# Kernel optimization log

Measured on AMD Instinct MI355X. Metric: run time of the kernel, lower is better.

## Reference

```python
import jax, jax.numpy as jnp
import numpy as np

N = 100_000   # nodes
E = 1_600_000 # edges
F_IN = 128
H = 128
C = 16


def setup_inputs() -> dict:
    key = jax.random.key(0)
    ks = jax.random.split(key, 11)
    s = 0.05
    return {
        "x": jax.random.normal(ks[0], (N, F_IN), jnp.float32),
        "edge_index": jax.random.randint(ks[1], (2, E), 0, N, jnp.int32),
        "edge_weight": jax.random.uniform(ks[2], (E,), jnp.float32),
        # first_lin: Linear(features_num, hidden)
        "W_first": jax.random.normal(ks[3], (F_IN, H), jnp.float32) * s,
        "b_first": jax.random.normal(ks[4], (H,), jnp.float32) * s,
        # two GCNConv(hidden, hidden) layers (num_layers - 1 = 2)
        "W_conv1": jax.random.normal(ks[5], (H, H), jnp.float32) * s,
        "b_conv1": jax.random.normal(ks[6], (H,), jnp.float32) * s,
        "W_conv2": jax.random.normal(ks[7], (H, H), jnp.float32) * s,
        "b_conv2": jax.random.normal(ks[8], (H,), jnp.float32) * s,
        # lin2: Linear(hidden, num_class)
        "W_out": jax.random.normal(ks[9], (H, C), jnp.float32) * s,
        "b_out": jax.random.normal(ks[10], (C,), jnp.float32) * s,
    }


def reference(x, edge_index, edge_weight, W_first, b_first,
              W_conv1, b_conv1, W_conv2, b_conv2, W_out, b_out):
    src, dst = edge_index[0], edge_index[1]

    # first_lin + relu (dropout p=0.8 is identity at inference)
    h = jax.nn.relu(x @ W_first + b_first)

    # GCN normalization with self-loops (fill weight 1.0), shared across layers
    deg = jax.ops.segment_sum(edge_weight, dst, num_segments=N) + 1.0
    dinv = jax.lax.rsqrt(deg)                      # [N]
    norm = dinv[src] * edge_weight * dinv[dst]     # [E]
    self_norm = dinv * dinv                        # [N], self-loop contribution

    for W, b in ((W_conv1, b_conv1), (W_conv2, b_conv2)):
        hw = h @ W                                  # [N, H]
        msgs = hw[src] * norm[:, None]              # [E, H] gather + scale
        agg = jax.ops.segment_sum(msgs, dst, num_segments=N)
        agg = agg + hw * self_norm[:, None]         # self-loop term
        h = jax.nn.relu(agg + b)

    # dropout p=0.5 identity at inference; final linear
    return h @ W_out + b_out
```

## Files before the change

kernel.cpp:

```cpp
#include <hip/hip_runtime.h>

typedef unsigned short u16;
typedef unsigned int u32;
using bf16x8 = __attribute__((ext_vector_type(8))) short;
using f32x4  = __attribute__((ext_vector_type(4))) float;

#define SLOT 64
#define NSHARD 128
#define SHMASK 127
#define SHBITS 7
#define QRT 4
#define SPQ 16
#define LDSN 782
#define CB 256
#define OVF_CAP 131072

static __device__ __forceinline__ u16 f2bf(float f) {
    u32 u = __float_as_uint(f);
    u = (u + 0x7fffu + ((u >> 16) & 1u)) >> 16;
    return (u16)u;
}
static __device__ __forceinline__ float bf2f(u16 h) {
    return __uint_as_float(((u32)h) << 16);
}
static __device__ __forceinline__ float pk_w(u32 e) {
    return (float)(int)((e & 0x7fffu) - 1u) * (1.0f / 32766.0f);
}
static __device__ __forceinline__ size_t nodeBase(int d) {
    return ((size_t)((d & SHMASK) * LDSN + (d >> SHBITS))) << 6;
}

__global__ void k_prep(const float* __restrict__ Wf, const float* __restrict__ W1,
                       const float* __restrict__ W2, u16* __restrict__ wfrag) {
    const float* W = (blockIdx.x == 0) ? Wf : (blockIdx.x == 1 ? W1 : W2);
    u16* o = wfrag + (size_t)blockIdx.x * 16384;
    for (int fid = threadIdx.x; fid < 2048; fid += 256) {
        int c = fid & 15, g = (fid >> 4) & 3, kk = (fid >> 6) & 3, ct = fid >> 8;
        const float* wp = W + (size_t)(kk * 32 + g * 8) * 128 + ct * 16 + c;
        bf16x8 pv;
#pragma unroll
        for (int j = 0; j < 8; ++j) pv[j] = (short)f2bf(wp[(size_t)j * 128]);
        *(bf16x8*)&o[(size_t)fid * 8] = pv;
    }
}

__global__ __launch_bounds__(256) void k_part1(const int* __restrict__ dst,
                                               int* __restrict__ cnt, int E, int CH) {
    __shared__ int lc[NSHARD];
    for (int i = threadIdx.x; i < NSHARD; i += 256) lc[i] = 0;
    __syncthreads();
    int e0 = blockIdx.x * CH, e1 = min(E, e0 + CH);
    for (int e = e0 + (int)threadIdx.x; e < e1; e += 256)
        atomicAdd(&lc[dst[e] & SHMASK], 1);
    __syncthreads();
    for (int i = threadIdx.x; i < NSHARD; i += 256)
        cnt[blockIdx.x * NSHARD + i] = lc[i];
}

__global__ __launch_bounds__(256) void k_scan_a(const int* __restrict__ cnt,
                                                int* __restrict__ offs,
                                                int* __restrict__ tot) {
    __shared__ int sd[256];
    int s = blockIdx.x, t = threadIdx.x;
    int v = cnt[t * NSHARD + s];
    sd[t] = v;
    __syncthreads();
    for (int off = 1; off < 256; off <<= 1) {
        int x = (t >= off) ? sd[t - off] : 0;
        __syncthreads();
        sd[t] += x;
        __syncthreads();
    }
    offs[s * CB + t] = sd[t] - v;
    if (t == 255) tot[s] = sd[255];
}

__global__ void k_scan_b(const int* __restrict__ tot, int* __restrict__ base, int E) {
    __shared__ int sd[NSHARD];
    int t = threadIdx.x;
    int v = tot[t];
    sd[t] = v;
    __syncthreads();
    for (int off = 1; off < NSHARD; off <<= 1) {
        int x = (t >= off) ? sd[t - off] : 0;
        __syncthreads();
        sd[t] += x;
        __syncthreads();
    }
    base[t] = sd[t] - v;
    if (t == NSHARD - 1) base[NSHARD] = E;
}

template <bool AF32, bool RELU_BIAS>
static __device__ __forceinline__ void gemm_body(
    int bid, const void* __restrict__ Araw, const u16* __restrict__ Wfrag,
    const float* __restrict__ bias, u16* __restrict__ C, int n)
{
    const int t = threadIdx.x;
    const int lane = t & 63;
    const int wave = t >> 6;
    const int rowbase = bid * 128 + wave * 32;
    const int lrow = lane & 15;
    const int g = lane >> 4;

    bf16x8 a[2][4];
#pragma unroll
    for (int rt = 0; rt < 2; ++rt) {
        int r = rowbase + rt * 16 + lrow;
        if (r < n) {
            if (AF32) {
                const float* ap = (const float*)Araw + (size_t)r * 128 + g * 8;
#pragma unroll
                for (int kki = 0; kki < 4; ++kki) {
                    float4 v0 = *(const float4*)(ap + kki * 32);
                    float4 v1 = *(const float4*)(ap + kki * 32 + 4);
                    bf16x8 av;
                    av[0] = (short)f2bf(v0.x);
                    av[1] = (short)f2bf(v0.y);
                    av[2] = (short)f2bf(v0.z);
                    av[3] = (short)f2bf(v0.w);
                    av[4] = (short)f2bf(v1.x);
                    av[5] = (short)f2bf(v1.y);
                    av[6] = (short)f2bf(v1.z);
                    av[7] = (short)f2bf(v1.w);
                    a[rt][kki] = av;
                }
            } else {
                const u16* ap = (const u16*)Araw + (size_t)r * 128 + g * 8;
#pragma unroll
                for (int kki = 0; kki < 4; ++kki)
                    a[rt][kki] = *(const bf16x8*)(ap + kki * 32);
            }
        } else {
#pragma unroll
            for (int kki = 0; kki < 4; ++kki)
                a[rt][kki] = (bf16x8)(short)0;
        }
    }

    f32x4 acc[2][8];
#pragma unroll
    for (int rt = 0; rt < 2; ++rt)
#pragma unroll
        for (int ct = 0; ct < 8; ++ct)
            acc[rt][ct] = (f32x4)0.0f;

#pragma unroll
    for (int ct = 0; ct < 8; ++ct) {
#pragma unroll
        for (int kki = 0; kki < 4; ++kki) {
            bf16x8 b = *(const bf16x8*)&Wfrag[((size_t)(ct * 4 + kki) * 64 + lane) * 8];
            acc[0][ct] = __builtin_amdgcn_mfma_f32_16x16x32_bf16(a[0][kki], b, acc[0][ct], 0, 0, 0);
            acc[1][ct] = __builtin_amdgcn_mfma_f32_16x16x32_bf16(a[1][kki], b, acc[1][ct], 0, 0, 0);
        }
    }

#pragma unroll
    for (int rt = 0; rt < 2; ++rt) {
#pragma unroll
        for (int ct = 0; ct < 8; ++ct) {
            int c = ct * 16 + lrow;
            float bv = 0.f;
            if (RELU_BIAS) bv = bias[c];
#pragma unroll
            for (int j = 0; j < 4; ++j) {
                int r = rowbase + rt * 16 + g * 4 + j;
                if (r < n) {
                    float v = acc[rt][ct][j];
                    if (RELU_BIAS) v = fmaxf(v + bv, 0.f);
                    C[(size_t)r * 128 + c] = f2bf(v);
                }
            }
        }
    }
}

__global__ __launch_bounds__(256) void kD(
    const int* __restrict__ src, const int* __restrict__ dst,
    const float* __restrict__ ew, const int* __restrict__ offs,
    const int* __restrict__ base, int2* __restrict__ part, int E, int CH,
    const float* __restrict__ x, const u16* __restrict__ wfragF,
    const float* __restrict__ bias, u16* __restrict__ C, int n)
{
    __shared__ int sbase[NSHARD];
    if ((int)blockIdx.x < CB) {
        int b = blockIdx.x, t = threadIdx.x;
        for (int i = t; i < NSHARD; i += 256) sbase[i] = base[i] + offs[i * CB + b];
        __syncthreads();
        int e0 = b * CH, e1 = min(E, e0 + CH);
        for (int e = e0 + t; e < e1; e += 256) {
            int d = dst[e];
            float w = ew[e];
            u32 w15 = 1u + (u32)fminf(w * 32766.0f + 0.5f, 32766.0f);
            u32 ent = ((u32)src[e] << 15) | w15;
            int pos = atomicAdd(&sbase[d & SHMASK], 1);
            part[pos] = make_int2(d, (int)ent);
        }
    } else {
        gemm_body<true, true>(blockIdx.x - CB, x, wfragF, bias, C, n);
    }
}

__global__ __launch_bounds__(256) void k_fill3(
    const int2* __restrict__ part, const int* __restrict__ base,
    u32* __restrict__ bucket, int2* __restrict__ ovf, int* __restrict__ ovf_cnt,
    int n)
{
    __shared__ u32 slots[LDSN * SPQ];
    __shared__ u32 cur[LDSN];
    const int s = blockIdx.x >> 2;
    const int q = blockIdx.x & 3;
    for (int i = threadIdx.x; i < LDSN * SPQ; i += 256) slots[i] = 0;
    for (int i = threadIdx.x; i < LDSN; i += 256) cur[i] = 0;
    __syncthreads();
    const int rb = base[s], re = base[s + 1];
    const int CHS = (re - rb + 3) >> 2;
    const int e0 = rb + q * CHS, e1 = min(re, e0 + CHS);
    for (int e = e0 + (int)threadIdx.x; e < e1; e += 256) {
        int2 v = part[e];
        int ln = v.x >> SHBITS;
        u32 p = atomicAdd(&cur[ln], 1u);
        if (p < SPQ) {
            slots[ln * SPQ + p] = (u32)v.y;
        } else {
            int g2 = atomicAdd(ovf_cnt, 1);
            if (g2 < OVF_CAP) ovf[g2] = v;
        }
    }
    __syncthreads();
    for (int i = threadIdx.x; i < LDSN * 4; i += 256) {
        int ln = i >> 2, k = i & 3;
        int d = (ln << SHBITS) + s;
        if (d < n) {
            u32* dp = bucket + nodeBase(d) + q * SPQ + k * 4;
            *(uint4*)dp = *(const uint4*)&slots[ln * SPQ + k * 4];
        }
    }
}

__global__ void k_fixup(u32* __restrict__ bucket, const int2* __restrict__ ovf,
                        const int* __restrict__ ovf_cnt) {
    int i = blockIdx.x * blockDim.x + threadIdx.x;
    int c = min(*ovf_cnt, OVF_CAP);
    if (i >= c) return;
    int2 v = ovf[i];
    u32* bp = bucket + nodeBase(v.x);
    for (int k = 0; k < SLOT; ++k) {
        if (bp[k] == 0u) {
            if (atomicCAS(&bp[k], 0u, (u32)v.y) == 0u) return;
        }
    }
}

static __device__ __forceinline__ void dinv_body(
    const u32* __restrict__ bucket, float* __restrict__ dinv, int n, int db)
{
    int node = db * 16 + (threadIdx.x >> 4);
    if (node >= n) return;
    int l = threadIdx.x & 15;
    const u32* bp = bucket + nodeBase(node);
    float sum = 0.f;
#pragma unroll
    for (int k = 0; k < 4; ++k) {
        u32 e = bp[l + k * 16];
        if (e) sum += pk_w(e);
    }
    sum += __shfl_xor(sum, 1);
    sum += __shfl_xor(sum, 2);
    sum += __shfl_xor(sum, 4);
    sum += __shfl_xor(sum, 8);
    if (l == 0) dinv[node] = rsqrtf(1.0f + sum);
}

__global__ __launch_bounds__(256) void kB(
    const u16* __restrict__ A, const u16* __restrict__ wfrag1,
    u16* __restrict__ C, int n, int G,
    const u32* __restrict__ bucket, float* __restrict__ dinv)
{
    if ((int)blockIdx.x < G)
        gemm_body<false, false>(blockIdx.x, A, wfrag1, nullptr, C, n);
    else
        dinv_body(bucket, dinv, n, blockIdx.x - G);
}

__global__ __launch_bounds__(256) void k_gemm(
    const u16* __restrict__ A, const u16* __restrict__ wfrag,
    u16* __restrict__ C, int n)
{
    gemm_body<false, false>(blockIdx.x, A, wfrag, nullptr, C, n);
}

template <bool FINAL>
__global__ __launch_bounds__(256) void k_gather_fin(
    const u16* __restrict__ hw, const u32* __restrict__ bucket,
    const float* __restrict__ dinv, const float* __restrict__ bias,
    u16* __restrict__ hout,
    const float* __restrict__ Wo, const float* __restrict__ bo,
    float* __restrict__ out, int n)
{
    __shared__ u32 comp[4][64];
    __shared__ float WoS[FINAL ? 2048 : 1];
    __shared__ float bos[FINAL ? 16 : 1];
    const int w = threadIdx.x >> 6;
    const int lane = threadIdx.x & 63;
    const int node = blockIdx.x * 4 + w;
    const bool active = node < n;

    if (FINAL) {
        for (int i = threadIdx.x; i < 2048; i += 256) WoS[i] = Wo[i];
        if (threadIdx.x < 16) bos[threadIdx.x] = bo[threadIdx.x];
    }

    u32 ent = 0;
    if (active) ent = bucket[nodeBase(node) + lane];
    unsigned long long mask = __ballot(ent != 0);
    int nv = __popcll(mask);
    int pos = __popcll(mask & ((1ull << lane) - 1ull));
    if (ent) comp[w][pos] = ent;
    __syncthreads();
    if (!active) return;

    const int grp = lane >> 4;
    const int gl = lane & 15;
    float acc[8] = {0.f, 0.f, 0.f, 0.f, 0.f, 0.f, 0.f, 0.f};
    int nit = (nv + 3) >> 2;
    int it = 0;
    for (; it + 1 < nit; it += 2) {
        int ka = it * 4 + grp;
        int kb = ka + 4;
        bool vb = kb < nv;
        u32 ea = comp[w][ka];
        u32 eb = comp[w][vb ? kb : 0];
        int sa = (int)(ea >> 15), sb = (int)(eb >> 15);
        bf16x8 ra = *(const bf16x8*)(hw + (size_t)sa * 128 + gl * 8);
        bf16x8 rb = *(const bf16x8*)(hw + (size_t)sb * 128 + gl * 8);
        float wa = dinv[sa] * pk_w(ea);
        float wb = vb ? dinv[sb] * pk_w(eb) : 0.f;
#pragma unroll
        for (int j = 0; j < 8; ++j) acc[j] = fmaf(wa, bf2f((u16)ra[j]), acc[j]);
#pragma unroll
        for (int j = 0; j < 8; ++j) acc[j] = fmaf(wb, bf2f((u16)rb[j]), acc[j]);
    }
    if (it < nit) {
        int ka = it * 4 + grp;
        bool va = ka < nv;
        u32 ea = comp[w][va ? ka : 0];
        int sa = (int)(ea >> 15);
        bf16x8 ra = *(const bf16x8*)(hw + (size_t)sa * 128 + gl * 8);
        float wa = va ? dinv[sa] * pk_w(ea) : 0.f;
#pragma unroll
        for (int j = 0; j < 8; ++j) acc[j] = fmaf(wa, bf2f((u16)ra[j]), acc[j]);
    }
#pragma unroll
    for (int j = 0; j < 8; ++j) {
        acc[j] += __shfl_xor(acc[j], 16);
        acc[j] += __shfl_xor(acc[j], 32);
    }

    float di = dinv[node];
    bf16x8 srow = *(const bf16x8*)(hw + (size_t)node * 128 + gl * 8);
    float4 b0 = *(const float4*)(bias + gl * 8);
    float4 b1 = *(const float4*)(bias + gl * 8 + 4);
    float bv[8] = {b0.x, b0.y, b0.z, b0.w, b1.x, b1.y, b1.z, b1.w};
    float hfin[8];
#pragma unroll
    for (int j = 0; j < 8; ++j)
        hfin[j] = fmaxf(fmaf(di, fmaf(di, bf2f((u16)srow[j]), acc[j]), bv[j]), 0.f);

    if (!FINAL) {
        if (grp == 0) {
            bf16x8 po;
#pragma unroll
            for (int j = 0; j < 8; ++j) po[j] = (short)f2bf(hfin[j]);
            *(bf16x8*)(hout + (size_t)node * 128 + gl * 8) = po;
        }
    } else {
        float partial = 0.f;
#pragma unroll
        for (int jj = 0; jj < 32; ++jj) {
            int j = grp * 32 + jj;
            float hj = __shfl(hfin[jj & 7], j >> 3);
            partial = fmaf(hj, WoS[j * 16 + gl], partial);
        }
        partial += __shfl_xor(partial, 16);
        partial += __shfl_xor(partial, 32);
        if (grp == 0) out[(size_t)node * 16 + gl] = partial + bos[gl];
    }
}

extern "C" void kernel_launch(void* const* d_in, const int* in_sizes, int n_in,
                              void* d_out, int out_size, void* d_ws, size_t ws_size,
                              hipStream_t stream) {
    const float* x  = (const float*)d_in[0];
    const int*   ei = (const int*)d_in[1];
    const float* ew = (const float*)d_in[2];
    const float* Wf = (const float*)d_in[3];
    const float* bf = (const float*)d_in[4];
    const float* W1 = (const float*)d_in[5];
    const float* b1 = (const float*)d_in[6];
    const float* W2 = (const float*)d_in[7];
    const float* b2 = (const float*)d_in[8];
    const float* Wo = (const float*)d_in[9];
    const float* bo = (const float*)d_in[10];
    float* out = (float*)d_out;

    const int N = in_sizes[0] / 128;
    const int E = in_sizes[2];
    const int* src = ei;
    const int* dst = ei + E;

    char* ws = (char*)d_ws;
    size_t off = 0;
    auto alloc = [&](size_t bytes) -> void* {
        void* p = ws + off;
        off = (off + bytes + 255) & ~(size_t)255;
        return p;
    };
    float* dinv    = (float*)alloc((size_t)N * 4);
    int*   ovf_cnt = (int*)alloc(256);
    int2*  ovf     = (int2*)alloc((size_t)OVF_CAP * 8);
    int*   cnt     = (int*)alloc((size_t)CB * NSHARD * 4);
    int*   offs    = (int*)alloc((size_t)NSHARD * CB * 4);
    int*   tot     = (int*)alloc((size_t)NSHARD * 4);
    int*   base    = (int*)alloc((size_t)(NSHARD + 1) * 4);
    u16*   wfrag   = (u16*)alloc((size_t)3 * 16384 * 2);
    int2*  part    = (int2*)alloc((size_t)E * 8);
    u32*   bucket  = (u32*)alloc((size_t)NSHARD * LDSN * SLOT * 4);
    u16*   bufA    = (u16*)alloc((size_t)N * 128 * 2);
    u16*   bufB    = (u16*)alloc((size_t)N * 128 * 2);
    (void)ws_size; (void)n_in; (void)out_size;

    const int G  = (N + 127) / 128;
    const int Db = (N + 15) / 16;
    const int gat_grid = (N + 3) / 4;
    const int CH = (E + CB - 1) / CB;

    hipMemsetAsync(ovf_cnt, 0, 4, stream);

    k_prep<<<3, 256, 0, stream>>>(Wf, W1, W2, wfrag);
    k_part1<<<CB, 256, 0, stream>>>(dst, cnt, E, CH);
    k_scan_a<<<NSHARD, 256, 0, stream>>>(cnt, offs, tot);
    k_scan_b<<<1, NSHARD, 0, stream>>>(tot, base, E);
    kD<<<CB + G, 256, 0, stream>>>(src, dst, ew, offs, base, part, E, CH,
                                   x, wfrag, bf, bufA, N);
    k_fill3<<<NSHARD * QRT, 256, 0, stream>>>(part, base, bucket, ovf, ovf_cnt, N);
    k_fixup<<<OVF_CAP / 256, 256, 0, stream>>>(bucket, ovf, ovf_cnt);
    kB<<<G + Db, 256, 0, stream>>>(bufA, wfrag + 16384, bufB, N, G, bucket, dinv);
    k_gather_fin<false><<<gat_grid, 256, 0, stream>>>(bufB, bucket, dinv, b1, bufA,
                                                      nullptr, nullptr, nullptr, N);
    k_gemm<<<G, 256, 0, stream>>>(bufA, wfrag + 32768, bufB, N);
    k_gather_fin<true><<<gat_grid, 256, 0, stream>>>(bufB, bucket, dinv, b2, nullptr,
                                                     Wo, bo, out, N);
}
```

Baseline: 269.9 us.

## Prescale GEMM outputs by dinv, compute degrees in fill, unroll gather

The source-side dinv factor now goes into the conv GEMM epilogue, so the gather no longer loads dinv[src] per edge. Degree sums are built in LDS during bucket filling, and a small kernel turns them into dinv, replacing the separate bucket scan fused with the GEMM. Weight prep is merged into the partition-count launch, the overflow fixup becomes grid-stride with fewer blocks, and the gather loop is unrolled four-deep with cheaper bf16 unpacking. The cost is an extra degree-partial buffer, an extra small kernel, and the first conv GEMM no longer overlapping with dinv work.

```diff
diff --git a/kernel.cpp b/kernel.cpp
--- a/kernel.cpp
+++ b/kernel.cpp
@@ -12,6 +12,7 @@
 #define QRT 4
 #define SPQ 16
 #define LDSN 782
+#define N1 (NSHARD * LDSN)
 #define CB 256
 #define OVF_CAP 131072
 
@@ -30,23 +31,26 @@
     return ((size_t)((d & SHMASK) * LDSN + (d >> SHBITS))) << 6;
 }
 
-__global__ void k_prep(const float* __restrict__ Wf, const float* __restrict__ W1,
-                       const float* __restrict__ W2, u16* __restrict__ wfrag) {
-    const float* W = (blockIdx.x == 0) ? Wf : (blockIdx.x == 1 ? W1 : W2);
-    u16* o = wfrag + (size_t)blockIdx.x * 16384;
-    for (int fid = threadIdx.x; fid < 2048; fid += 256) {
-        int c = fid & 15, g = (fid >> 4) & 3, kk = (fid >> 6) & 3, ct = fid >> 8;
-        const float* wp = W + (size_t)(kk * 32 + g * 8) * 128 + ct * 16 + c;
-        bf16x8 pv;
-#pragma unroll
-        for (int j = 0; j < 8; ++j) pv[j] = (short)f2bf(wp[(size_t)j * 128]);
-        *(bf16x8*)&o[(size_t)fid * 8] = pv;
-    }
-}
-
-__global__ __launch_bounds__(256) void k_part1(const int* __restrict__ dst,
-                                               int* __restrict__ cnt, int E, int CH) {
+__global__ __launch_bounds__(256) void k_part1(
+    const int* __restrict__ dst, int* __restrict__ cnt, int E, int CH,
+    const float* __restrict__ Wf, const float* __restrict__ W1,
+    const float* __restrict__ W2, u16* __restrict__ wfrag)
+{
     __shared__ int lc[NSHARD];
+    if ((int)blockIdx.x >= CB) {
+        int m = blockIdx.x - CB;
+        const float* W = (m == 0) ? Wf : (m == 1 ? W1 : W2);
+        u16* o = wfrag + (size_t)m * 16384;
+        for (int fid = threadIdx.x; fid < 2048; fid += 256) {
+            int c = fid & 15, g = (fid >> 4) & 3, kk = (fid >> 6) & 3, ct = fid >> 8;
+            const float* wp = W + (size_t)(kk * 32 + g * 8) * 128 + ct * 16 + c;
+            bf16x8 pv;
+#pragma unroll
+            for (int j = 0; j < 8; ++j) pv[j] = (short)f2bf(wp[(size_t)j * 128]);
+            *(bf16x8*)&o[(size_t)fid * 8] = pv;
+        }
+        return;
+    }
     for (int i = threadIdx.x; i < NSHARD; i += 256) lc[i] = 0;
     __syncthreads();
     int e0 = blockIdx.x * CH, e1 = min(E, e0 + CH);
@@ -91,10 +95,11 @@
     if (t == NSHARD - 1) base[NSHARD] = E;
 }
 
-template <bool AF32, bool RELU_BIAS>
+template <bool AF32, bool RELU_BIAS, bool SCALE>
 static __device__ __forceinline__ void gemm_body(
     int bid, const void* __restrict__ Araw, const u16* __restrict__ Wfrag,
-    const float* __restrict__ bias, u16* __restrict__ C, int n)
+    const float* __restrict__ bias, const float* __restrict__ dinv,
+    u16* __restrict__ C, int n)
 {
     const int t = threadIdx.x;
     const int lane = t & 63;
@@ -138,6 +143,17 @@
         }
     }
 
+    float dv[2][4];
+    if (SCALE) {
+#pragma unroll
+        for (int rt = 0; rt < 2; ++rt)
+#pragma unroll
+            for (int j = 0; j < 4; ++j) {
+                int r = rowbase + rt * 16 + g * 4 + j;
+                dv[rt][j] = (r < n) ? dinv[r] : 0.f;
+            }
+    }
+
     f32x4 acc[2][8];
 #pragma unroll
     for (int rt = 0; rt < 2; ++rt)
@@ -167,6 +183,7 @@
                 int r = rowbase + rt * 16 + g * 4 + j;
                 if (r < n) {
                     float v = acc[rt][ct][j];
+                    if (SCALE) v *= dv[rt][j];
                     if (RELU_BIAS) v = fmaxf(v + bv, 0.f);
                     C[(size_t)r * 128 + c] = f2bf(v);
                 }
@@ -197,21 +214,22 @@
             part[pos] = make_int2(d, (int)ent);
         }
     } else {
-        gemm_body<true, true>(blockIdx.x - CB, x, wfragF, bias, C, n);
+        gemm_body<true, true, false>(blockIdx.x - CB, x, wfragF, bias, nullptr, C, n);
     }
 }
 
 __global__ __launch_bounds__(256) void k_fill3(
     const int2* __restrict__ part, const int* __restrict__ base,
-    u32* __restrict__ bucket, int2* __restrict__ ovf, int* __restrict__ ovf_cnt,
-    int n)
+    u32* __restrict__ bucket, float* __restrict__ degp,
+    int2* __restrict__ ovf, int* __restrict__ ovf_cnt, int n)
 {
     __shared__ u32 slots[LDSN * SPQ];
     __shared__ u32 cur[LDSN];
+    __shared__ u32 lideg[LDSN];
     const int s = blockIdx.x >> 2;
     const int q = blockIdx.x & 3;
     for (int i = threadIdx.x; i < LDSN * SPQ; i += 256) slots[i] = 0;
-    for (int i = threadIdx.x; i < LDSN; i += 256) cur[i] = 0;
+    for (int i = threadIdx.x; i < LDSN; i += 256) { cur[i] = 0; lideg[i] = 0; }
     __syncthreads();
     const int rb = base[s], re = base[s + 1];
     const int CHS = (re - rb + 3) >> 2;
@@ -219,6 +237,7 @@
     for (int e = e0 + (int)threadIdx.x; e < e1; e += 256) {
         int2 v = part[e];
         int ln = v.x >> SHBITS;
+        atomicAdd(&lideg[ln], ((u32)v.y & 0x7fffu) - 1u);
         u32 p = atomicAdd(&cur[ln], 1u);
         if (p < SPQ) {
             slots[ln * SPQ + p] = (u32)v.y;
@@ -236,58 +255,41 @@
             *(uint4*)dp = *(const uint4*)&slots[ln * SPQ + k * 4];
         }
     }
+    for (int i = threadIdx.x; i < LDSN; i += 256)
+        degp[(size_t)q * N1 + s * LDSN + i] = (float)lideg[i] * (1.0f / 32766.0f);
 }
 
 __global__ void k_fixup(u32* __restrict__ bucket, const int2* __restrict__ ovf,
                         const int* __restrict__ ovf_cnt) {
-    int i = blockIdx.x * blockDim.x + threadIdx.x;
     int c = min(*ovf_cnt, OVF_CAP);
-    if (i >= c) return;
-    int2 v = ovf[i];
-    u32* bp = bucket + nodeBase(v.x);
-    for (int k = 0; k < SLOT; ++k) {
-        if (bp[k] == 0u) {
-            if (atomicCAS(&bp[k], 0u, (u32)v.y) == 0u) return;
-        }
-    }
-}
-
-static __device__ __forceinline__ void dinv_body(
-    const u32* __restrict__ bucket, float* __restrict__ dinv, int n, int db)
-{
-    int node = db * 16 + (threadIdx.x >> 4);
-    if (node >= n) return;
-    int l = threadIdx.x & 15;
-    const u32* bp = bucket + nodeBase(node);
-    float sum = 0.f;
-#pragma unroll
-    for (int k = 0; k < 4; ++k) {
-        u32 e = bp[l + k * 16];
-        if (e) sum += pk_w(e);
-    }
-    sum += __shfl_xor(sum, 1);
-    sum += __shfl_xor(sum, 2);
-    sum += __shfl_xor(sum, 4);
-    sum += __shfl_xor(sum, 8);
-    if (l == 0) dinv[node] = rsqrtf(1.0f + sum);
-}
-
-__global__ __launch_bounds__(256) void kB(
-    const u16* __restrict__ A, const u16* __restrict__ wfrag1,
-    u16* __restrict__ C, int n, int G,
-    const u32* __restrict__ bucket, float* __restrict__ dinv)
-{
-    if ((int)blockIdx.x < G)
-        gemm_body<false, false>(blockIdx.x, A, wfrag1, nullptr, C, n);
-    else
-        dinv_body(bucket, dinv, n, blockIdx.x - G);
+    for (int i = blockIdx.x * blockDim.x + threadIdx.x; i < c;
+         i += gridDim.x * blockDim.x) {
+        int2 v = ovf[i];
+        u32* bp = bucket + nodeBase(v.x);
+        for (int k = 0; k < SLOT; ++k) {
+            if (bp[k] == 0u) {
+                if (atomicCAS(&bp[k], 0u, (u32)v.y) == 0u) break;
+            }
+        }
+    }
+}
+
+__global__ __launch_bounds__(256) void k_dinv2(const float* __restrict__ degp,
+                                               float* __restrict__ dinv, int n) {
+    int i = blockIdx.x * 256 + threadIdx.x;
+    if (i >= N1) return;
+    int s = i / LDSN, ln = i - s * LDSN;
+    int d = (ln << SHBITS) + s;
+    if (d >= n) return;
+    float sum = degp[i] + degp[N1 + i] + degp[2 * N1 + i] + degp[3 * N1 + i];
+    dinv[d] = rsqrtf(1.0f + sum);
 }
 
 __global__ __launch_bounds__(256) void k_gemm(
     const u16* __restrict__ A, const u16* __restrict__ wfrag,
-    u16* __restrict__ C, int n)
-{
-    gemm_body<false, false>(blockIdx.x, A, wfrag, nullptr, C, n);
+    const float* __restrict__ dinv, u16* __restrict__ C, int n)
+{
+    gemm_body<false, false, true>(blockIdx.x, A, wfrag, nullptr, dinv, C, n);
 }
 
 template <bool FINAL>
@@ -322,35 +324,50 @@
 
     const int grp = lane >> 4;
     const int gl = lane & 15;
+    const u32* cw = comp[w];
     float acc[8] = {0.f, 0.f, 0.f, 0.f, 0.f, 0.f, 0.f, 0.f};
-    int nit = (nv + 3) >> 2;
-    int it = 0;
-    for (; it + 1 < nit; it += 2) {
-        int ka = it * 4 + grp;
-        int kb = ka + 4;
-        bool vb = kb < nv;
-        u32 ea = comp[w][ka];
-        u32 eb = comp[w][vb ? kb : 0];
-        int sa = (int)(ea >> 15), sb = (int)(eb >> 15);
-        bf16x8 ra = *(const bf16x8*)(hw + (size_t)sa * 128 + gl * 8);
-        bf16x8 rb = *(const bf16x8*)(hw + (size_t)sb * 128 + gl * 8);
-        float wa = dinv[sa] * pk_w(ea);
-        float wb = vb ? dinv[sb] * pk_w(eb) : 0.f;
-#pragma unroll
-        for (int j = 0; j < 8; ++j) acc[j] = fmaf(wa, bf2f((u16)ra[j]), acc[j]);
-#pragma unroll
-        for (int j = 0; j < 8; ++j) acc[j] = fmaf(wb, bf2f((u16)rb[j]), acc[j]);
-    }
-    if (it < nit) {
-        int ka = it * 4 + grp;
-        bool va = ka < nv;
-        u32 ea = comp[w][va ? ka : 0];
-        int sa = (int)(ea >> 15);
-        bf16x8 ra = *(const bf16x8*)(hw + (size_t)sa * 128 + gl * 8);
-        float wa = va ? dinv[sa] * pk_w(ea) : 0.f;
-#pragma unroll
-        for (int j = 0; j < 8; ++j) acc[j] = fmaf(wa, bf2f((u16)ra[j]), acc[j]);
-    }
+
+    auto fma8 = [&](float ww, const bf16x8& rr) {
+        const u32* qq = (const u32*)&rr;
+#pragma unroll
+        for (int k = 0; k < 4; ++k) {
+            u32 u = qq[k];
+            acc[2 * k]     = fmaf(ww, __uint_as_float(u << 16), acc[2 * k]);
+            acc[2 * k + 1] = fmaf(ww, __uint_as_float(u & 0xffff0000u), acc[2 * k + 1]);
+        }
+    };
+
+    if (nv > 0) {
+        int full = nv >> 2;
+        int it = 0;
+        for (; it + 4 <= full; it += 4) {
+            u32 e0 = cw[(it + 0) * 4 + grp];
+            u32 e1 = cw[(it + 1) * 4 + grp];
+            u32 e2 = cw[(it + 2) * 4 + grp];
+            u32 e3 = cw[(it + 3) * 4 + grp];
+            bf16x8 r0 = *(const bf16x8*)(hw + (size_t)(e0 >> 15) * 128 + gl * 8);
+            bf16x8 r1 = *(const bf16x8*)(hw + (size_t)(e1 >> 15) * 128 + gl * 8);
+            bf16x8 r2 = *(const bf16x8*)(hw + (size_t)(e2 >> 15) * 128 + gl * 8);
+            bf16x8 r3 = *(const bf16x8*)(hw + (size_t)(e3 >> 15) * 128 + gl * 8);
+            fma8(pk_w(e0), r0);
+            fma8(pk_w(e1), r1);
+            fma8(pk_w(e2), r2);
+            fma8(pk_w(e3), r3);
+        }
+        for (; it < full; ++it) {
+            u32 e0 = cw[it * 4 + grp];
+            bf16x8 r0 = *(const bf16x8*)(hw + (size_t)(e0 >> 15) * 128 + gl * 8);
+            fma8(pk_w(e0), r0);
+        }
+        int idx = full * 4 + grp;
+        if (full * 4 < nv) {
+            bool va = idx < nv;
+            u32 e0 = cw[va ? idx : 0];
+            bf16x8 r0 = *(const bf16x8*)(hw + (size_t)(e0 >> 15) * 128 + gl * 8);
+            fma8(va ? pk_w(e0) : 0.f, r0);
+        }
+    }
+
 #pragma unroll
     for (int j = 0; j < 8; ++j) {
         acc[j] += __shfl_xor(acc[j], 16);
@@ -365,7 +382,7 @@
     float hfin[8];
 #pragma unroll
     for (int j = 0; j < 8; ++j)
-        hfin[j] = fmaxf(fmaf(di, fmaf(di, bf2f((u16)srow[j]), acc[j]), bv[j]), 0.f);
+        hfin[j] = fmaxf(fmaf(di, acc[j] + bf2f((u16)srow[j]), bv[j]), 0.f);
 
     if (!FINAL) {
         if (grp == 0) {
@@ -424,31 +441,31 @@
     int*   tot     = (int*)alloc((size_t)NSHARD * 4);
     int*   base    = (int*)alloc((size_t)(NSHARD + 1) * 4);
     u16*   wfrag   = (u16*)alloc((size_t)3 * 16384 * 2);
+    float* degp    = (float*)alloc((size_t)4 * N1 * 4);
     int2*  part    = (int2*)alloc((size_t)E * 8);
-    u32*   bucket  = (u32*)alloc((size_t)NSHARD * LDSN * SLOT * 4);
+    u32*   bucket  = (u32*)alloc((size_t)N1 * SLOT * 4);
     u16*   bufA    = (u16*)alloc((size_t)N * 128 * 2);
     u16*   bufB    = (u16*)alloc((size_t)N * 128 * 2);
     (void)ws_size; (void)n_in; (void)out_size;
 
     const int G  = (N + 127) / 128;
-    const int Db = (N + 15) / 16;
     const int gat_grid = (N + 3) / 4;
     const int CH = (E + CB - 1) / CB;
 
     hipMemsetAsync(ovf_cnt, 0, 4, stream);
 
-    k_prep<<<3, 256, 0, stream>>>(Wf, W1, W2, wfrag);
-    k_part1<<<CB, 256, 0, stream>>>(dst, cnt, E, CH);
+    k_part1<<<CB + 3, 256, 0, stream>>>(dst, cnt, E, CH, Wf, W1, W2, wfrag);
     k_scan_a<<<NSHARD, 256, 0, stream>>>(cnt, offs, tot);
     k_scan_b<<<1, NSHARD, 0, stream>>>(tot, base, E);
     kD<<<CB + G, 256, 0, stream>>>(src, dst, ew, offs, base, part, E, CH,
                                    x, wfrag, bf, bufA, N);
-    k_fill3<<<NSHARD * QRT, 256, 0, stream>>>(part, base, bucket, ovf, ovf_cnt, N);
-    k_fixup<<<OVF_CAP / 256, 256, 0, stream>>>(bucket, ovf, ovf_cnt);
-    kB<<<G + Db, 256, 0, stream>>>(bufA, wfrag + 16384, bufB, N, G, bucket, dinv);
+    k_fill3<<<NSHARD * QRT, 256, 0, stream>>>(part, base, bucket, degp, ovf, ovf_cnt, N);
+    k_fixup<<<16, 256, 0, stream>>>(bucket, ovf, ovf_cnt);
+    k_dinv2<<<(N1 + 255) / 256, 256, 0, stream>>>(degp, dinv, N);
+    k_gemm<<<G, 256, 0, stream>>>(bufA, wfrag + 16384, dinv, bufB, N);
     k_gather_fin<false><<<gat_grid, 256, 0, stream>>>(bufB, bucket, dinv, b1, bufA,
                                                       nullptr, nullptr, nullptr, N);
-    k_gemm<<<G, 256, 0, stream>>>(bufA, wfrag + 32768, bufB, N);
+    k_gemm<<<G, 256, 0, stream>>>(bufA, wfrag + 32768, dinv, bufB, N);
     k_gather_fin<true><<<gat_grid, 256, 0, stream>>>(bufB, bucket, dinv, b2, nullptr,
                                                      Wo, bo, out, N);
 }
```

Result: no change. 266.1 us (-1.4%).
